# Optimization experiments

Measured on AMD Instinct MI355X. Metric: run time of the kernel, lower is better.

## Reference

```python
import jax, jax.numpy as jnp
import numpy as np


def setup_inputs() -> dict:
    key = jax.random.key(0)
    ks = jax.random.split(key, 7)
    N, E, din, dout, de = 4096, 16384, 1024, 1024, 3
    H_v = jax.random.normal(ks[0], (N, din), dtype=jnp.float32)
    edge_features = jax.random.normal(ks[1], (E, de), dtype=jnp.float32)
    adj_v = jax.random.uniform(ks[2], (N, N), dtype=jnp.float32)
    T = jax.random.uniform(ks[3], (N, E), dtype=jnp.float32)
    weight = jax.random.normal(ks[4], (din, dout), dtype=jnp.float32) * (1.0 / np.sqrt(dout))
    bias = jax.random.normal(ks[5], (dout,), dtype=jnp.float32) * (1.0 / np.sqrt(dout))
    p = jax.random.normal(ks[6], (1, de), dtype=jnp.float32)
    return {"H_v": H_v, "edge_features": edge_features, "adj_v": adj_v, "T": T,
            "weight": weight, "bias": bias, "p": p}


def reference(H_v, edge_features, adj_v, T, weight, bias, p):
    # w[e] = (edge_features @ p^T)[e]  -- per-edge scalar weight
    w = (edge_features @ p.T)[:, 0]                     # [E]
    # T @ diag(w) @ T^T  computed as column-scaled T times T^T  -> [N, N]
    multiplier = (T * w[None, :]) @ T.T                 # [N, N]
    N = multiplier.shape[0]
    eye = jnp.eye(N, dtype=multiplier.dtype)
    # M: ones on the diagonal, multiplier off-diagonal
    M = eye + (1.0 - eye) * multiplier
    adjusted_A = M * adj_v                              # [N, N]
    out = adjusted_A @ (H_v @ weight) + bias            # [N, dout]
    return out
```

## Files before the change

kernel.cpp:

```cpp
#include <hip/hip_runtime.h>
#include <hip/hip_bf16.h>
#include <stdint.h>

typedef __attribute__((ext_vector_type(4))) float f32x4;
typedef __attribute__((ext_vector_type(8))) short bf16x8;
typedef __attribute__((ext_vector_type(4))) unsigned short u16x4;

static __device__ __forceinline__ unsigned short f2bf(float f) {
    __hip_bfloat16 h = __float2bfloat16(f);
    return *reinterpret_cast<unsigned short*>(&h);
}

static __device__ __forceinline__ void gload_lds16(const void* g, void* l) {
    __builtin_amdgcn_global_load_lds(
        (const __attribute__((address_space(1))) unsigned int*)(uintptr_t)g,
        (__attribute__((address_space(3))) unsigned int*)(uintptr_t)l,
        16, 0, 0);
}

__global__ void calc_w(const float* __restrict__ ef, const float* __restrict__ p,
                       float* __restrict__ w, int E) {
    int e = blockIdx.x * 256 + threadIdx.x;
    if (e < E) w[e] = ef[3*e] * p[0] + ef[3*e+1] * p[1] + ef[3*e+2] * p[2];
}

__global__ void conv_T(const float* __restrict__ T, const float* __restrict__ wbuf,
                       __hip_bfloat16* __restrict__ Aw, __hip_bfloat16* __restrict__ Bt,
                       size_t total4, int E, unsigned int emask) {
    size_t i = (size_t)blockIdx.x * blockDim.x + threadIdx.x;
    size_t stride = (size_t)gridDim.x * blockDim.x;
    for (; i < total4; i += stride) {
        size_t base = i * 4;
        float4 t = reinterpret_cast<const float4*>(T)[i];
        int c = (emask != 0xFFFFFFFFu) ? (int)(base & (size_t)emask)
                                       : (int)(base % (size_t)E);
        float w0 = wbuf[c], w1 = wbuf[c+1], w2 = wbuf[c+2], w3 = wbuf[c+3];
        u16x4 b, a;
        b[0] = f2bf(t.x); b[1] = f2bf(t.y); b[2] = f2bf(t.z); b[3] = f2bf(t.w);
        a[0] = f2bf(t.x * w0); a[1] = f2bf(t.y * w1); a[2] = f2bf(t.z * w2); a[3] = f2bf(t.w * w3);
        reinterpret_cast<u16x4*>(Bt)[i] = b;
        reinterpret_cast<u16x4*>(Aw)[i] = a;
    }
}

__global__ void conv_plain(const float* __restrict__ src, __hip_bfloat16* __restrict__ dst,
                           size_t total4) {
    size_t i = (size_t)blockIdx.x * blockDim.x + threadIdx.x;
    size_t stride = (size_t)gridDim.x * blockDim.x;
    for (; i < total4; i += stride) {
        float4 t = reinterpret_cast<const float4*>(src)[i];
        u16x4 b;
        b[0] = f2bf(t.x); b[1] = f2bf(t.y); b[2] = f2bf(t.z); b[3] = f2bf(t.w);
        reinterpret_cast<u16x4*>(dst)[i] = b;
    }
}

__global__ void conv_Wt(const float* __restrict__ Wsrc, __hip_bfloat16* __restrict__ Wt,
                        int din, int dout) {
    int idx = blockIdx.x * 256 + threadIdx.x;
    if (idx < din * dout) {
        int i = idx / dout, j = idx % dout;
        Wt[(size_t)j * din + i] = __float2bfloat16(Wsrc[idx]);
    }
}

template <int EPI>
__global__ __launch_bounds__(256)
void gemm_bt(const __hip_bfloat16* __restrict__ A, const __hip_bfloat16* __restrict__ B,
             int M, int Ng, int K,
             const float* __restrict__ adj, float* __restrict__ outF,
             const float* __restrict__ bias, __hip_bfloat16* __restrict__ outB, int ldT) {
    constexpr int BM = 128, BN = 128, BK = 64;
    __shared__ __align__(16) __hip_bfloat16 As[2][BM * BK];
    __shared__ __align__(16) __hip_bfloat16 Bs[2][BN * BK];

    const int tid  = threadIdx.x;
    const int lane = tid & 63;
    const int wv   = tid >> 6;
    const int wr   = wv >> 1, wc = wv & 1;

    int b = blockIdx.x;
    const int nwg = gridDim.x;
    if ((nwg & 7) == 0) {
        const int q = nwg >> 3;
        b = (b & 7) * q + (b >> 3);
    }
    const int nbx = Ng / BN;
    const int bx = b % nbx, by = b / nbx;
    const int row0 = by * BM, col0 = bx * BN;

    f32x4 acc[4][4] = {};

    const int frow = lane & 15;
    const int hi   = lane >> 4;
    const int r7   = frow & 7;

    const int NT = K / BK;

    auto stage = [&](int t, int bufi) {
        const int k0 = t * BK;
        #pragma unroll
        for (int it = 0; it < 4; ++it) {
            const int chunkW = it * 256 + wv * 64;
            const int chunk  = chunkW + lane;
            const int r  = chunk >> 3;
            const int jj = chunk & 7;
            const int c  = (jj ^ (r & 7)) * 8;
            gload_lds16(A + (size_t)(row0 + r) * K + k0 + c, (void*)(&As[bufi][chunkW * 8]));
            gload_lds16(B + (size_t)(col0 + r) * K + k0 + c, (void*)(&Bs[bufi][chunkW * 8]));
        }
    };

    stage(0, 0);
    __syncthreads();

    for (int t = 0; t < NT; ++t) {
        if (t + 1 < NT) stage(t + 1, (t + 1) & 1);
        const int bufi = t & 1;
        #pragma unroll
        for (int kk = 0; kk < 2; ++kk) {
            const int co = ((kk * 4 + hi) ^ r7) * 8;
            bf16x8 af[4], bfr[4];
            #pragma unroll
            for (int m = 0; m < 4; ++m)
                af[m] = *reinterpret_cast<const bf16x8*>(
                    &As[bufi][(wr * 64 + m * 16 + frow) * BK + co]);
            #pragma unroll
            for (int n = 0; n < 4; ++n)
                bfr[n] = *reinterpret_cast<const bf16x8*>(
                    &Bs[bufi][(wc * 64 + n * 16 + frow) * BK + co]);
            #pragma unroll
            for (int m = 0; m < 4; ++m)
                #pragma unroll
                for (int n = 0; n < 4; ++n)
                    acc[m][n] = __builtin_amdgcn_mfma_f32_16x16x32_bf16(
                        af[m], bfr[n], acc[m][n], 0, 0, 0);
        }
        __syncthreads();
    }

    const int rbase  = row0 + wr * 64 + (lane >> 4) * 4;
    const int cbase2 = col0 + wc * 64 + (lane & 15);
    #pragma unroll
    for (int m = 0; m < 4; ++m) {
        #pragma unroll
        for (int n = 0; n < 4; ++n) {
            const int col = cbase2 + n * 16;
            if constexpr (EPI == 3) {
                u16x4 pk;
                #pragma unroll
                for (int i = 0; i < 4; ++i) pk[i] = f2bf(acc[m][n][i]);
                *reinterpret_cast<u16x4*>(&outB[(size_t)col * ldT + rbase + m * 16]) = pk;
            } else {
                #pragma unroll
                for (int i = 0; i < 4; ++i) {
                    const int row = rbase + m * 16 + i;
                    const size_t idx = (size_t)row * Ng + col;
                    if constexpr (EPI == 1) {
                        float a = adj[idx];
                        float v = (row == col) ? a : acc[m][n][i] * a;
                        outB[idx] = __float2bfloat16(v);
                    } else {
                        outF[idx] = acc[m][n][i] + bias[col];
                    }
                }
            }
        }
    }
}

extern "C" void kernel_launch(void* const* d_in, const int* in_sizes, int n_in,
                              void* d_out, int out_size, void* d_ws, size_t ws_size,
                              hipStream_t stream) {
    const float* H_v  = (const float*)d_in[0];
    const float* ef   = (const float*)d_in[1];
    const float* adj  = (const float*)d_in[2];
    const float* T    = (const float*)d_in[3];
    const float* Wght = (const float*)d_in[4];
    const float* bias = (const float*)d_in[5];
    const float* p    = (const float*)d_in[6];
    float* out = (float*)d_out;

    const int dout = in_sizes[5];
    const int din  = in_sizes[4] / dout;
    const int N    = in_sizes[0] / din;
    const int E    = in_sizes[1] / 3;

    auto align256 = [](size_t x) { return (x + 255) & ~(size_t)255; };
    size_t off = 0;
    size_t off_w    = off; off = align256(off + (size_t)E * 4);
    size_t off_A    = off; off = align256(off + (size_t)N * E * 2);
    size_t off_B    = off; off = align256(off + (size_t)N * E * 2);
    size_t off_adjA = off; off = align256(off + (size_t)N * N * 2);
    size_t off_Hb   = off; off = align256(off + (size_t)N * din * 2);
    size_t off_Wt   = off; off = align256(off + (size_t)din * dout * 2);
    size_t off_HWt  = off; off = align256(off + (size_t)dout * N * 2);
    if (ws_size < off) return;

    char* ws = (char*)d_ws;
    float* w_f = (float*)(ws + off_w);
    __hip_bfloat16* Aw   = (__hip_bfloat16*)(ws + off_A);
    __hip_bfloat16* Bt   = (__hip_bfloat16*)(ws + off_B);
    __hip_bfloat16* adjA = (__hip_bfloat16*)(ws + off_adjA);
    __hip_bfloat16* Hb   = (__hip_bfloat16*)(ws + off_Hb);
    __hip_bfloat16* Wt   = (__hip_bfloat16*)(ws + off_Wt);
    __hip_bfloat16* HWt  = (__hip_bfloat16*)(ws + off_HWt);

    const unsigned int emask = ((E & (E - 1)) == 0) ? (unsigned int)(E - 1) : 0xFFFFFFFFu;

    calc_w<<<(E + 255) / 256, 256, 0, stream>>>(ef, p, w_f, E);
    conv_T<<<2048, 256, 0, stream>>>(T, w_f, Aw, Bt, (size_t)N * E / 4, E, emask);
    conv_plain<<<1024, 256, 0, stream>>>(H_v, Hb, (size_t)N * din / 4);
    conv_Wt<<<(din * dout + 255) / 256, 256, 0, stream>>>(Wght, Wt, din, dout);
    gemm_bt<3><<<(N / 128) * (dout / 128), 256, 0, stream>>>(
        Hb, Wt, N, dout, din, nullptr, nullptr, nullptr, HWt, N);
    gemm_bt<1><<<(N / 128) * (N / 128), 256, 0, stream>>>(
        Aw, Bt, N, N, E, adj, nullptr, nullptr, adjA, 0);
    gemm_bt<2><<<(N / 128) * (dout / 128), 256, 0, stream>>>(
        adjA, HWt, N, dout, N, nullptr, out, bias, nullptr, 0);
}
```

Before: 1.250 ms.

## Use 256x256-tile 8-wave GEMM with split staging for the T·diag(w)·Tᵀ product

Adds a new gemm8_bt kernel with 256x256 output tiles, 512 threads (8 waves), and an 8x4 MFMA accumulator per wave. It is used for the dominant N×N×E multiplier GEMM. Prefetch of the next K tile is split into halves interleaved with the MFMA phases, and the kernel uses explicit waitcnt/barrier control plus s_setprio. The larger tiles are meant to raise arithmetic intensity and cut global traffic, and the software pipelining is meant to overlap loads with compute. In exchange it uses 128KB of LDS, only 256 workgroups, and fragile manual vmcnt counting.

```diff
diff --git a/kernel.cpp b/kernel.cpp
--- a/kernel.cpp
+++ b/kernel.cpp
@@ -94,8 +94,7 @@
     const int frow = lane & 15;
     const int hi   = lane >> 4;
     const int r7   = frow & 7;
-
-    const int NT = K / BK;
+    const int NT   = K / BK;
 
     auto stage = [&](int t, int bufi) {
         const int k0 = t * BK;
@@ -139,8 +138,8 @@
         __syncthreads();
     }
 
-    const int rbase  = row0 + wr * 64 + (lane >> 4) * 4;
-    const int cbase2 = col0 + wc * 64 + (lane & 15);
+    const int rbase  = row0 + wr * 64 + hi * 4;
+    const int cbase2 = col0 + wc * 64 + frow;
     #pragma unroll
     for (int m = 0; m < 4; ++m) {
         #pragma unroll
@@ -169,6 +168,147 @@
     }
 }
 
+template <int EPI>
+__global__ __launch_bounds__(512)
+void gemm8_bt(const __hip_bfloat16* __restrict__ A, const __hip_bfloat16* __restrict__ B,
+              int M, int Ng, int K,
+              const float* __restrict__ adj, float* __restrict__ outF,
+              const float* __restrict__ bias, __hip_bfloat16* __restrict__ outB, int ldT) {
+    constexpr int BM = 256, BN = 256, BK = 64;
+    __shared__ __align__(16) __hip_bfloat16 As[2][2 * 8192];
+    __shared__ __align__(16) __hip_bfloat16 Bs[2][2 * 8192];
+
+    const int tid  = threadIdx.x;
+    const int lane = tid & 63;
+    const int wid  = tid >> 6;
+    const int wr   = wid >> 2;
+    const int wc   = wid & 3;
+
+    int b = blockIdx.x;
+    const int nwg = gridDim.x;
+    if ((nwg & 7) == 0) {
+        const int q = nwg >> 3;
+        b = (b & 7) * q + (b >> 3);
+    }
+    const int nbx = Ng / BN;
+    const int bx = b % nbx, by = b / nbx;
+    const int row0 = by * BM, col0 = bx * BN;
+
+    f32x4 acc[8][4] = {};
+
+    const int frow = lane & 15;
+    const int hi   = lane >> 4;
+    const int r7   = frow & 7;
+    const int NT   = K / BK;
+
+    auto stage_half = [&](int t, int dbuf, int part) {
+        const int k0 = t * BK;
+        const __hip_bfloat16* src = (part < 2) ? A : B;
+        const int base0 = (part < 2) ? row0 : col0;
+        const int h = part & 1;
+        __hip_bfloat16* dst = (part < 2) ? &As[dbuf][h * 8192] : &Bs[dbuf][h * 8192];
+        #pragma unroll
+        for (int it = 0; it < 2; ++it) {
+            const int chunkW = it * 512 + (tid & ~63);
+            const int chunk  = chunkW + lane;
+            const int r  = chunk >> 3;
+            const int jj = chunk & 7;
+            const int c  = (jj ^ (r & 7)) * 8;
+            gload_lds16(src + (size_t)(base0 + h * 128 + r) * K + k0 + c,
+                        (void*)(dst + chunkW * 8));
+        }
+    };
+
+    stage_half(0, 0, 0); stage_half(0, 0, 1); stage_half(0, 0, 2); stage_half(0, 0, 3);
+
+    for (int t = 0; t < NT; ++t) {
+        const int d = t & 1;
+        if (t + 1 < NT) {
+            stage_half(t + 1, d ^ 1, 0);
+            stage_half(t + 1, d ^ 1, 1);
+            asm volatile("s_waitcnt vmcnt(4)" ::: "memory");
+        } else {
+            asm volatile("s_waitcnt vmcnt(0)" ::: "memory");
+        }
+        __builtin_amdgcn_s_barrier();
+        __builtin_amdgcn_sched_barrier(0);
+
+        bf16x8 af[4][2];
+        #pragma unroll
+        for (int p = 0; p < 4; ++p) {
+            const int mh = p >> 1, nh = p & 1;
+            if (nh == 0) {
+                #pragma unroll
+                for (int mm = 0; mm < 4; ++mm)
+                    #pragma unroll
+                    for (int kk = 0; kk < 2; ++kk) {
+                        const int row = (mh * 4 + mm) * 16 + frow;
+                        const int co  = ((kk * 4 + hi) ^ r7) * 8;
+                        af[mm][kk] = *reinterpret_cast<const bf16x8*>(
+                            &As[d][wr * 8192 + row * 64 + co]);
+                    }
+            }
+            bf16x8 bq[2][2];
+            #pragma unroll
+            for (int nn = 0; nn < 2; ++nn)
+                #pragma unroll
+                for (int kk = 0; kk < 2; ++kk) {
+                    const int row = (wc & 1) * 64 + (nh * 2 + nn) * 16 + frow;
+                    const int co  = ((kk * 4 + hi) ^ r7) * 8;
+                    bq[nn][kk] = *reinterpret_cast<const bf16x8*>(
+                        &Bs[d][(wc >> 1) * 8192 + row * 64 + co]);
+                }
+            if (p == 1 && t + 1 < NT) {
+                stage_half(t + 1, d ^ 1, 2);
+                stage_half(t + 1, d ^ 1, 3);
+            }
+            __builtin_amdgcn_s_barrier();
+            asm volatile("s_waitcnt lgkmcnt(0)");
+            __builtin_amdgcn_s_setprio(1);
+            #pragma unroll
+            for (int mm = 0; mm < 4; ++mm)
+                #pragma unroll
+                for (int nn = 0; nn < 2; ++nn)
+                    #pragma unroll
+                    for (int kk = 0; kk < 2; ++kk)
+                        acc[mh * 4 + mm][nh * 2 + nn] =
+                            __builtin_amdgcn_mfma_f32_16x16x32_bf16(
+                                af[mm][kk], bq[nn][kk], acc[mh * 4 + mm][nh * 2 + nn], 0, 0, 0);
+            __builtin_amdgcn_s_setprio(0);
+            __builtin_amdgcn_s_barrier();
+        }
+    }
+
+    const int rbase  = row0 + wr * 128 + hi * 4;
+    const int cbase2 = col0 + wc * 64 + frow;
+    #pragma unroll
+    for (int m = 0; m < 8; ++m) {
+        #pragma unroll
+        for (int n = 0; n < 4; ++n) {
+            const int col = cbase2 + n * 16;
+            if constexpr (EPI == 3) {
+                u16x4 pk;
+                #pragma unroll
+                for (int i = 0; i < 4; ++i) pk[i] = f2bf(acc[m][n][i]);
+                *reinterpret_cast<u16x4*>(&outB[(size_t)col * ldT + rbase + m * 16]) = pk;
+            } else {
+                #pragma unroll
+                for (int i = 0; i < 4; ++i) {
+                    const int row = rbase + m * 16 + i;
+                    const size_t idx = (size_t)row * Ng + col;
+                    if constexpr (EPI == 1) {
+                        float a = adj[idx];
+                        float v = (row == col) ? a : acc[m][n][i] * a;
+                        outB[idx] = __float2bfloat16(v);
+                    } else {
+                        outF[idx] = acc[m][n][i] + bias[col];
+                    }
+                }
+            }
+        }
+    }
+}
+
 extern "C" void kernel_launch(void* const* d_in, const int* in_sizes, int n_in,
                               void* d_out, int out_size, void* d_ws, size_t ws_size,
                               hipStream_t stream) {
@@ -214,7 +354,7 @@
     conv_Wt<<<(din * dout + 255) / 256, 256, 0, stream>>>(Wght, Wt, din, dout);
     gemm_bt<3><<<(N / 128) * (dout / 128), 256, 0, stream>>>(
         Hb, Wt, N, dout, din, nullptr, nullptr, nullptr, HWt, N);
-    gemm_bt<1><<<(N / 128) * (N / 128), 256, 0, stream>>>(
+    gemm8_bt<1><<<(N / 256) * (N / 256), 512, 0, stream>>>(
         Aw, Bt, N, N, E, adj, nullptr, nullptr, adjA, 0);
     gemm_bt<2><<<(N / 128) * (dout / 128), 256, 0, stream>>>(
         adjA, HWt, N, dout, N, nullptr, out, bias, nullptr, 0);
```

New measurement: 1.020 ms. 1.23x faster.
